# Kernel tuning notes

Hardware: AMD Instinct MI355X
Metric: run time of the kernel (lower is better)

The kernel has to match this reference:

```python
import jax, jax.numpy as jnp
import numpy as np
from jax import lax

BIG = 1e10  # initial distance, matching torch's 1e10


def farthest_point_sample(xyz, init_farthest, npoint):
    """xyz: [B,N,3] float; init_farthest: [B] int32; returns centroids [B,npoint] int32."""
    B, N, _ = xyz.shape
    batch_idx = jnp.arange(B)

    def body(i, state):
        centroids, distance, farthest = state
        centroids = centroids.at[:, i].set(farthest)
        c = xyz[batch_idx, farthest][:, None, :]              # [B,1,3] current centroid
        dist = jnp.sum(jnp.square(xyz - c), axis=-1)          # [B,N] sq. distance
        distance = jnp.minimum(distance, dist)                # mask-update: keep min dist to any centroid
        farthest = jnp.argmax(distance, axis=-1).astype(jnp.int32)
        return centroids, distance, farthest

    centroids0 = jnp.zeros((B, npoint), jnp.int32)
    distance0 = jnp.full((B, N), BIG, xyz.dtype)
    centroids, _, _ = lax.fori_loop(0, npoint, body, (centroids0, distance0, init_farthest.astype(jnp.int32)))
    return centroids


def setup_inputs() -> dict:
    key = jax.random.key(0)
    k1, k2, k3 = jax.random.split(key, 3)
    B, N = 16, 100000
    mesh = jax.random.normal(k1, (B, N, 3), dtype=jnp.float32)
    contact_map = jax.random.uniform(k2, (B, N, 1), dtype=jnp.float32)
    init_farthest = jax.random.randint(k3, (B,), 0, N, dtype=jnp.int32)
    return {"mesh": mesh, "contact_map": contact_map, "init_farthest": init_farthest, "npoint": 1024}


def reference(mesh, contact_map, init_farthest, npoint):
    B, N, _ = mesh.shape
    batch_idx = jnp.arange(B)

    # __compute_mesh_scale: max distance from centroid, per batch
    centroid = jnp.mean(mesh, axis=1, keepdims=True)                      # [B,1,3]
    s_obj = jnp.max(jnp.sqrt(jnp.sum(jnp.square(mesh - centroid), axis=2)), axis=1)  # [B]

    # __farthest_point_sample
    centroids = farthest_point_sample(mesh, init_farthest, npoint)        # [B,npoint]

    # gather sampled points and contact values
    point_cloud = mesh[batch_idx[:, None], centroids]                     # [B,npoint,3]
    cm_sampled = contact_map[batch_idx[:, None], centroids]               # [B,npoint,1]

    # normalize by object scale (broadcast over points/coords)
    point_cloud_norm = point_cloud / s_obj[:, None, None]

    # point_cloud_norm_contact fed to the contact encoder in the original
    return jnp.concatenate([cm_sampled, point_cloud_norm], axis=2)        # [B,npoint,4]
```

## Files before the change

kernel.cpp:

```cpp
#include <hip/hip_runtime.h>
#include <cstdint>

#define NBATCH 16
#define NPOINT 1024
#define NPTS   100000
#define GPB    16
#define TPB    256
#define WPB    4
#define NSUB   16
#define STRIDE (GPB * TPB)
#define KPT    25
#define NPAIR  13

typedef unsigned long long u64;


__global__ __launch_bounds__(256) void sum_kernel(const float* __restrict__ xyz,
                                                  float* __restrict__ psum) {
    const int b   = blockIdx.x & 15;
    const int sub = blockIdx.x >> 4;
    const float* P = xyz + (size_t)b * NPTS * 3;
    float sx = 0.f, sy = 0.f, sz = 0.f;
    for (int i = sub * TPB + threadIdx.x; i < NPTS; i += NSUB * TPB) {
        sx += P[i * 3 + 0];
        sy += P[i * 3 + 1];
        sz += P[i * 3 + 2];
    }
    #pragma unroll
    for (int off = 32; off; off >>= 1) {
        sx += __shfl_xor(sx, off);
        sy += __shfl_xor(sy, off);
        sz += __shfl_xor(sz, off);
    }
    __shared__ float r[3][4];
    const int wave = threadIdx.x >> 6, lane = threadIdx.x & 63;
    if (lane == 0) { r[0][wave] = sx; r[1][wave] = sy; r[2][wave] = sz; }
    __syncthreads();
    if (threadIdx.x == 0) {
        float* o = psum + (b * NSUB + sub) * 4;
        o[0] = r[0][0] + r[0][1] + r[0][2] + r[0][3];
        o[1] = r[1][0] + r[1][1] + r[1][2] + r[1][3];
        o[2] = r[2][0] + r[2][1] + r[2][2] + r[2][3];
    }
}

__global__ __launch_bounds__(256) void max_kernel(const float* __restrict__ xyz,
                                                  const float* __restrict__ psum,
                                                  unsigned* __restrict__ pmax,
                                                  u64* __restrict__ slots) {
    if (blockIdx.x == 0) {
        slots[threadIdx.x] = 0ull;
        slots[threadIdx.x + 256] = 0ull;
    }
    const int b   = blockIdx.x & 15;
    const int sub = blockIdx.x >> 4;
    const float* P = xyz + (size_t)b * NPTS * 3;
    float sx = 0.f, sy = 0.f, sz = 0.f;
    #pragma unroll
    for (int s = 0; s < NSUB; ++s) {
        sx += psum[(b * NSUB + s) * 4 + 0];
        sy += psum[(b * NSUB + s) * 4 + 1];
        sz += psum[(b * NSUB + s) * 4 + 2];
    }
    const float mx = sx / (float)NPTS, my = sy / (float)NPTS, mz = sz / (float)NPTS;
    float best = 0.f;
    for (int i = sub * TPB + threadIdx.x; i < NPTS; i += NSUB * TPB) {
        float dx = P[i * 3 + 0] - mx;
        float dy = P[i * 3 + 1] - my;
        float dz = P[i * 3 + 2] - mz;
        best = fmaxf(best, dx * dx + dy * dy + dz * dz);
    }
    #pragma unroll
    for (int off = 32; off; off >>= 1) best = fmaxf(best, __shfl_xor(best, off));
    __shared__ float r[4];
    const int wave = threadIdx.x >> 6, lane = threadIdx.x & 63;
    if (lane == 0) r[wave] = best;
    __syncthreads();
    if (threadIdx.x == 0)
        pmax[b * NSUB + sub] = __float_as_uint(fmaxf(fmaxf(r[0], r[1]), fmaxf(r[2], r[3])));
}

__global__ __launch_bounds__(256, 1) void fps_kernel(const float* __restrict__ xyz,
                                                     const float* __restrict__ cmap,
                                                     const int* __restrict__ init_far,
                                                     const unsigned* __restrict__ pmax,
                                                     u64* __restrict__ slots,
                                                     float* __restrict__ out) {
    const int b   = blockIdx.x & 15;
    const int g   = blockIdx.x >> 4;
    const int tid = threadIdx.x;
    const int wave = tid >> 6, lane = tid & 63;
    const int tl  = g * TPB + tid;
    const float* P = xyz + (size_t)b * NPTS * 3;

    float m0 = 0.f;
    #pragma unroll
    for (int s = 0; s < NSUB; ++s) m0 = fmaxf(m0, __uint_as_float(pmax[b * NSUB + s]));
    const float sb = sqrtf(m0);

    float pxx[NPAIR], pxy[NPAIR], pyx[NPAIR], pyy[NPAIR],
          pzx[NPAIR], pzy[NPAIR], pdx[NPAIR], pdy[NPAIR];
    #pragma unroll
    for (int j = 0; j < NPAIR; ++j) {
        const int p0 = tl + (2 * j) * STRIDE;
        const int p1 = tl + (2 * j + 1) * STRIDE;
        const bool v0 = p0 < NPTS, v1 = p1 < NPTS;
        pxx[j] = v0 ? P[p0 * 3 + 0] : 0.f;  pxy[j] = v1 ? P[p1 * 3 + 0] : 0.f;
        pyx[j] = v0 ? P[p0 * 3 + 1] : 0.f;  pyy[j] = v1 ? P[p1 * 3 + 1] : 0.f;
        pzx[j] = v0 ? P[p0 * 3 + 2] : 0.f;  pzy[j] = v1 ? P[p1 * 3 + 2] : 0.f;
        pdx[j] = v0 ? 1e10f : -1.0f;        pdy[j] = v1 ? 1e10f : -1.0f;
    }

    __shared__ u64   lds_key[WPB];
    __shared__ int   lds_win;
    __shared__ float lds_x, lds_y, lds_z;
    __shared__ int   curhist[NPOINT];

    int cur = init_far[b];
    float cx = P[cur * 3 + 0], cy = P[cur * 3 + 1], cz = P[cur * 3 + 2];

    for (int i = 0; i < NPOINT; ++i) {
        if (tid == 192) curhist[i] = cur;
        if (i == NPOINT - 1) break;

        float best = -1.0f;
        int bidx = 0;
        {
            #pragma clang fp contract(off)
            #pragma unroll
            for (int j = 0; j < NPAIR; ++j) {
                float dx0 = pxx[j] - cx, dx1 = pxy[j] - cx;
                float dy0 = pyx[j] - cy, dy1 = pyy[j] - cy;
                float dz0 = pzx[j] - cz, dz1 = pzy[j] - cz;
                float s0 = dx0 * dx0 + dy0 * dy0;  float s1 = dx1 * dx1 + dy1 * dy1;
                s0 = s0 + dz0 * dz0;               s1 = s1 + dz1 * dz1;
                float n0 = fminf(pdx[j], s0);      float n1 = fminf(pdy[j], s1);
                pdx[j] = n0;                       pdy[j] = n1;
                if (n0 > best) { best = n0; bidx = tl + (2 * j) * STRIDE; }
                if (n1 > best) { best = n1; bidx = tl + (2 * j + 1) * STRIDE; }
            }
        }

        const u64 want = (u64)(i + 1);
        u64 key = ((u64)__float_as_uint(best) << 22) | (u64)(0x3FFFFFu - (unsigned)bidx);
        #pragma unroll
        for (int off = 32; off; off >>= 1) {
            u64 o2 = __shfl_xor(key, off);
            key = o2 > key ? o2 : key;
        }
        if (lane == 0) lds_key[wave] = key;
        __syncthreads();

        u64* const bs = slots + ((size_t)(i & 1) * NBATCH + b) * GPB;

        if (wave == 0) {
            u64 bk = (lane < WPB) ? lds_key[lane] : 0;
            #pragma unroll
            for (int off = 1; off < WPB; off <<= 1) {
                u64 o2 = __shfl_xor(bk, off);
                bk = o2 > bk ? o2 : bk;
            }
            if (lane == 0)
                __hip_atomic_store(&bs[g], bk | (want << 54),
                                   __ATOMIC_RELAXED, __HIP_MEMORY_SCOPE_AGENT);
        }

        u64 v = 0;
        int ci = 0;
        float gx = 0.f, gy = 0.f, gz = 0.f;
        if (lane < GPB) {
            u64* sp = &bs[lane];
            int tries = 0;
            for (;;) {
                v = __hip_atomic_load(sp, __ATOMIC_RELAXED, __HIP_MEMORY_SCOPE_AGENT);
                if ((v >> 54) >= want) break;
                if (++tries > 64) __builtin_amdgcn_s_sleep(1);
            }
            ci = (int)(0x3FFFFFu - (unsigned)(v & 0x3FFFFFu));
            gx = P[ci * 3 + 0];
            gy = P[ci * 3 + 1];
            gz = P[ci * 3 + 2];
        }
        u64 kk = v;
        #pragma unroll
        for (int off = 8; off; off >>= 1) {
            u64 o2 = __shfl_xor(kk, off);
            kk = o2 > kk ? o2 : kk;
        }
        if (lane < GPB && v == kk) {
            lds_win = ci;
            lds_x = gx; lds_y = gy; lds_z = gz;
        }
        __syncthreads();
        cur = lds_win;
        cx = lds_x; cy = lds_y; cz = lds_z;
    }

    __syncthreads();
    if (tid < 64) {
        const int row = g * 64 + tid;
        const int c   = curhist[row];
        const float cm = cmap[(size_t)b * NPTS + c];
        const float x = P[c * 3 + 0], y = P[c * 3 + 1], z = P[c * 3 + 2];
        float* o = out + ((size_t)b * NPOINT + row) * 4;
        o[0] = cm;
        o[1] = x / sb;
        o[2] = y / sb;
        o[3] = z / sb;
    }
}

extern "C" void kernel_launch(void* const* d_in, const int* in_sizes, int n_in,
                              void* d_out, int out_size, void* d_ws, size_t ws_size,
                              hipStream_t stream) {
    const float* mesh = (const float*)d_in[0];
    const float* cmap = (const float*)d_in[1];
    const int* init   = (const int*)d_in[2];
    float* out = (float*)d_out;

    char* ws      = (char*)d_ws;
    float* psum   = (float*)ws;
    unsigned* pmx = (unsigned*)(ws + 4096);
    u64* slots    = (u64*)(ws + 8192);

    sum_kernel<<<dim3(256), dim3(TPB), 0, stream>>>(mesh, psum);
    max_kernel<<<dim3(256), dim3(TPB), 0, stream>>>(mesh, psum, pmx, slots);
    fps_kernel<<<dim3(256), dim3(TPB), 0, stream>>>(mesh, cmap, init, pmx, slots, out);
}
```

Before: 2.012 ms.

## Replace per-iteration block barriers with LDS flag-based wave handoff

Removes both __syncthreads per FPS iteration. Waves now publish their argmax keys to double-buffered LDS slots tagged with the iteration number. Wave 0 spins on those slots, does the cross-block global exchange alone, and broadcasts the winning centroid through tagged LDS words that the other waves poll. This takes barrier latency off the serial critical path, but non-zero waves now busy-spin on LDS. The sleep backoff in the global poll is also lowered from 64 to 16 tries.

```diff
diff --git a/kernel.cpp b/kernel.cpp
--- a/kernel.cpp
+++ b/kernel.cpp
@@ -111,10 +111,13 @@
         pdx[j] = v0 ? 1e10f : -1.0f;        pdy[j] = v1 ? 1e10f : -1.0f;
     }
 
-    __shared__ u64   lds_key[WPB];
-    __shared__ int   lds_win;
-    __shared__ float lds_x, lds_y, lds_z;
-    __shared__ int   curhist[NPOINT];
+    __shared__ u64 wkey[2][WPB];
+    __shared__ u64 wres[2][4];
+    __shared__ int curhist[NPOINT];
+
+    if (tid < 8)  wkey[tid >> 2][tid & 3] = 0ull;
+    if (tid >= 8 && tid < 16) wres[(tid - 8) >> 2][tid & 3] = 0ull;
+    __syncthreads();
 
     int cur = init_far[b];
     float cx = P[cur * 3 + 0], cy = P[cur * 3 + 1], cz = P[cur * 3 + 2];
@@ -142,58 +145,96 @@
         }
 
         const u64 want = (u64)(i + 1);
+        const unsigned want32 = (unsigned)want;
         u64 key = ((u64)__float_as_uint(best) << 22) | (u64)(0x3FFFFFu - (unsigned)bidx);
         #pragma unroll
         for (int off = 32; off; off >>= 1) {
             u64 o2 = __shfl_xor(key, off);
             key = o2 > key ? o2 : key;
         }
-        if (lane == 0) lds_key[wave] = key;
-        __syncthreads();
+
+        u64* const wk = &wkey[i & 1][0];
+        if (lane == 0)
+            __hip_atomic_store(&wk[wave], key | (want << 54),
+                               __ATOMIC_RELAXED, __HIP_MEMORY_SCOPE_WORKGROUP);
 
         u64* const bs = slots + ((size_t)(i & 1) * NBATCH + b) * GPB;
 
         if (wave == 0) {
-            u64 bk = (lane < WPB) ? lds_key[lane] : 0;
+            u64 kv = 0;
+            if (lane < WPB) {
+                for (;;) {
+                    kv = __hip_atomic_load(&wk[lane], __ATOMIC_RELAXED,
+                                           __HIP_MEMORY_SCOPE_WORKGROUP);
+                    if ((kv >> 54) >= want) break;
+                }
+            }
+            u64 bk = kv;
             #pragma unroll
             for (int off = 1; off < WPB; off <<= 1) {
                 u64 o2 = __shfl_xor(bk, off);
                 bk = o2 > bk ? o2 : bk;
             }
             if (lane == 0)
-                __hip_atomic_store(&bs[g], bk | (want << 54),
+                __hip_atomic_store(&bs[g], (bk & 0x003FFFFFFFFFFFFFull) | (want << 54),
                                    __ATOMIC_RELAXED, __HIP_MEMORY_SCOPE_AGENT);
+
+            u64 v = 0;
+            if (lane < GPB) {
+                u64* sp = &bs[lane];
+                int tries = 0;
+                for (;;) {
+                    v = __hip_atomic_load(sp, __ATOMIC_RELAXED, __HIP_MEMORY_SCOPE_AGENT);
+                    if ((v >> 54) >= want) break;
+                    if (++tries > 16) __builtin_amdgcn_s_sleep(1);
+                }
+            }
+            const int ci = (int)(0x3FFFFFu - (unsigned)(v & 0x3FFFFFu));
+            float gx = 0.f, gy = 0.f, gz = 0.f;
+            if (lane < GPB) {
+                gx = P[ci * 3 + 0];
+                gy = P[ci * 3 + 1];
+                gz = P[ci * 3 + 2];
+            }
+            u64 kk = v;
+            #pragma unroll
+            for (int off = 8; off; off >>= 1) {
+                u64 o2 = __shfl_xor(kk, off);
+                kk = o2 > kk ? o2 : kk;
+            }
+            const bool win = (lane < GPB) && (v == kk);
+            if (win) {
+                u64* wr = &wres[i & 1][0];
+                __hip_atomic_store(&wr[0], (u64)(unsigned)ci | ((u64)want32 << 32),
+                                   __ATOMIC_RELAXED, __HIP_MEMORY_SCOPE_WORKGROUP);
+                __hip_atomic_store(&wr[1], (u64)__float_as_uint(gx) | ((u64)want32 << 32),
+                                   __ATOMIC_RELAXED, __HIP_MEMORY_SCOPE_WORKGROUP);
+                __hip_atomic_store(&wr[2], (u64)__float_as_uint(gy) | ((u64)want32 << 32),
+                                   __ATOMIC_RELAXED, __HIP_MEMORY_SCOPE_WORKGROUP);
+                __hip_atomic_store(&wr[3], (u64)__float_as_uint(gz) | ((u64)want32 << 32),
+                                   __ATOMIC_RELAXED, __HIP_MEMORY_SCOPE_WORKGROUP);
+            }
+            const int wl = __ffsll(__ballot(win)) - 1;
+            cur = __shfl(ci, wl);
+            cx  = __shfl(gx, wl);
+            cy  = __shfl(gy, wl);
+            cz  = __shfl(gz, wl);
+        } else {
+            u64 r = 0;
+            if (lane < 4) {
+                u64* wr = &wres[i & 1][0];
+                for (;;) {
+                    r = __hip_atomic_load(&wr[lane], __ATOMIC_RELAXED,
+                                          __HIP_MEMORY_SCOPE_WORKGROUP);
+                    if ((unsigned)(r >> 32) == want32) break;
+                }
+            }
+            const unsigned lo = (unsigned)r;
+            cur = (int)__shfl((int)lo, 0);
+            cx  = __uint_as_float(__shfl(lo, 1));
+            cy  = __uint_as_float(__shfl(lo, 2));
+            cz  = __uint_as_float(__shfl(lo, 3));
         }
-
-        u64 v = 0;
-        int ci = 0;
-        float gx = 0.f, gy = 0.f, gz = 0.f;
-        if (lane < GPB) {
-            u64* sp = &bs[lane];
-            int tries = 0;
-            for (;;) {
-                v = __hip_atomic_load(sp, __ATOMIC_RELAXED, __HIP_MEMORY_SCOPE_AGENT);
-                if ((v >> 54) >= want) break;
-                if (++tries > 64) __builtin_amdgcn_s_sleep(1);
-            }
-            ci = (int)(0x3FFFFFu - (unsigned)(v & 0x3FFFFFu));
-            gx = P[ci * 3 + 0];
-            gy = P[ci * 3 + 1];
-            gz = P[ci * 3 + 2];
-        }
-        u64 kk = v;
-        #pragma unroll
-        for (int off = 8; off; off >>= 1) {
-            u64 o2 = __shfl_xor(kk, off);
-            kk = o2 > kk ? o2 : kk;
-        }
-        if (lane < GPB && v == kk) {
-            lds_win = ci;
-            lds_x = gx; lds_y = gy; lds_z = gz;
-        }
-        __syncthreads();
-        cur = lds_win;
-        cx = lds_x; cy = lds_y; cz = lds_z;
     }
 
     __syncthreads();
```

Result: slower. 2.058 ms (+2.3%).
